# Optimization experiments

Hardware: AMD Instinct MI355X
Metric: run time of the kernel (lower is better)

The kernel has to match this reference:

```python
import jax, jax.numpy as jnp
from jax import lax
import numpy as np

C = 256
K = 3
PAD = 1


def _bilinear_sample(x, py, px):
    """Zero-padded bilinear sampling.
    x: [B,C,Hin,Win]; py,px: [B,Kt,H,W] float sample coords -> [B,C,Kt,H,W]."""
    B, Cc, Hin, Win = x.shape
    y0 = jnp.floor(py)
    x0 = jnp.floor(px)
    y1 = y0 + 1.0
    x1 = x0 + 1.0
    wy1 = py - y0
    wy0 = 1.0 - wy1
    wx1 = px - x0
    wx0 = 1.0 - wx1
    xf = x.reshape(B, Cc, Hin * Win)

    def corner(yi, xi, wy, wx):
        valid = (yi >= 0) & (yi < Hin) & (xi >= 0) & (xi < Win)
        yc = jnp.clip(yi, 0, Hin - 1).astype(jnp.int32)
        xc = jnp.clip(xi, 0, Win - 1).astype(jnp.int32)
        idx = yc * Win + xc  # [B,Kt,H,W]
        g = jax.vmap(lambda xb, ib: xb[:, ib])(xf, idx)  # [B,C,Kt,H,W]
        w = (wy * wx) * valid.astype(x.dtype)
        return g * w[:, None]

    return (corner(y0, x0, wy0, wx0) + corner(y0, x1, wy0, wx1)
            + corner(y1, x0, wy1, wx0) + corner(y1, x1, wy1, wx1))


def _arm_forward(x, w_off, b_off, w, b):
    B, Cc, H, W = x.shape
    # offset-predicting conv (standard 3x3, pad 1)
    off = lax.conv_general_dilated(
        x, w_off, window_strides=(1, 1), padding=[(PAD, PAD), (PAD, PAD)],
        dimension_numbers=('NCHW', 'OIHW', 'NCHW')) + b_off[None, :, None, None]
    off = off.reshape(B, K * K, 2, H, W)  # [:, k, 0]=dy, [:, k, 1]=dx (mmcv layout)
    ky, kx = jnp.meshgrid(jnp.arange(K), jnp.arange(K), indexing='ij')
    ky = ky.reshape(-1).astype(x.dtype)  # [9]
    kx = kx.reshape(-1).astype(x.dtype)
    base_y = jnp.arange(H, dtype=x.dtype)[None, None, :, None]
    base_x = jnp.arange(W, dtype=x.dtype)[None, None, None, :]
    py = base_y - PAD + ky[None, :, None, None] + off[:, :, 0]  # [B,9,H,W]
    px = base_x - PAD + kx[None, :, None, None] + off[:, :, 1]
    sampled = _bilinear_sample(x, py, px)  # [B,C,9,H,W]
    out = jnp.einsum('bckhw,ock->bohw', sampled, w.reshape(Cc, Cc, K * K))
    out = out + b[None, :, None, None]
    return jax.nn.sigmoid(out)


def setup_inputs() -> dict:
    key = jax.random.key(0)
    k1, k2, k3, k4 = jax.random.split(key, 4)
    B, H, W = 8, 64, 64
    x = jax.random.normal(k1, (B, C, H, W), dtype=jnp.float32)
    # offset conv params (mmcv zero-inits these; use small random to exercise sampling)
    w_off = jax.random.normal(k2, (2 * K * K, C, K, K), dtype=jnp.float32) * 0.01
    b_off = jnp.zeros((2 * K * K,), dtype=jnp.float32)
    # deformable conv weight/bias (kaiming-ish scale)
    scale = 1.0 / np.sqrt(C * K * K)
    w = jax.random.normal(k3, (C, C, K, K), dtype=jnp.float32) * scale
    b = jax.random.normal(k4, (C,), dtype=jnp.float32) * scale
    return {"Fstagei": x, "w_off": w_off, "b_off": b_off, "w": w, "b": b}


def reference(Fstagei, w_off, b_off, w, b):
    return _arm_forward(Fstagei, w_off, b_off, w, b)
```

## Files before the change

kernel.cpp:

```cpp
#include <hip/hip_runtime.h>

typedef unsigned short u16;
typedef unsigned int u32;
typedef __attribute__((ext_vector_type(8))) short short8;
typedef __attribute__((ext_vector_type(4))) float f32x4;

#define BB 8
#define CCH 256
#define HH 64
#define WW 64
#define HP 66
#define NPOS 4096
#define KTOT 2304

#define XT_BYTES   17842176ull
#define W2R_OFF    17842176ull
#define WOFF2_OFF  19021824ull
#define OFF2_OFF   40402944ull
#define WS_MIN     42762240ull

__device__ __forceinline__ u16 f2bf(float f) {
    union { float f; u32 u; } v; v.f = f;
    u32 r = v.u + 0x7FFFu + ((v.u >> 16) & 1u);
    return (u16)(r >> 16);
}
__device__ __forceinline__ u32 pk2(float a, float b) {
    return (u32)f2bf(a) | ((u32)f2bf(b) << 16);
}
__device__ __forceinline__ u32 cvtpk(float lo, float hi) {
    u32 r;
    asm("v_cvt_pk_bf16_f32 %0, %1, %2" : "=v"(r) : "v"(lo), "v"(hi));
    return r;
}
__device__ __forceinline__ void bf2x2(u32 p, float& a, float& b) {
    union { u32 u; float f; } va, vb;
    va.u = p << 16; vb.u = p & 0xffff0000u;
    a = va.f; b = vb.f;
}
__device__ __forceinline__ void ldg_lds16(const u16* g, u16* l) {
    __builtin_amdgcn_global_load_lds((const __attribute__((address_space(1))) u32*)g,
                                     (__attribute__((address_space(3))) u32*)l, 16, 0, 0);
}

__global__ __launch_bounds__(256) void k_pre(const float* __restrict__ w, const float* __restrict__ w_off,
                                             const float* __restrict__ x,
                                             u16* __restrict__ W2r, u16* __restrict__ Woff2,
                                             u16* __restrict__ xT) {
    __shared__ __align__(16) float SH[4608];
    int bx = blockIdx.x;
    int t = threadIdx.x;
    if (bx < 256) {
        int o = bx;
        const float* src = w + (size_t)o * 2304;
#pragma unroll
        for (int j = 0; j < 9; ++j) SH[j * 256 + t] = src[j * 256 + t];
        __syncthreads();
        u16* dst = W2r + (size_t)o * 2304;
#pragma unroll
        for (int k = 0; k < 9; ++k) dst[k * 256 + t] = f2bf(SH[t * 9 + k]);
    } else if (bx == 256) {
        for (int o2 = 0; o2 < 32; ++o2) {
            if (o2 < 18) {
                const float* src = w_off + (size_t)o2 * 2304;
#pragma unroll
                for (int j = 0; j < 9; ++j) SH[j * 256 + t] = src[j * 256 + t];
                __syncthreads();
#pragma unroll
                for (int k = 0; k < 9; ++k) Woff2[(size_t)o2 * 2304 + k * 256 + t] = f2bf(SH[t * 9 + k]);
                __syncthreads();
            } else {
#pragma unroll
                for (int k = 0; k < 9; ++k) Woff2[(size_t)o2 * 2304 + k * 256 + t] = 0;
            }
        }
    } else if (bx < 777) {
        int idx = (bx - 257) * 4 + (t >> 6);
        int b = idx / 260, m = idx - b * 260;
        int y, xx;
        if (m < 66)       { y = 0;  xx = m; }
        else if (m < 132) { y = 65; xx = m - 66; }
        else if (m < 196) { y = m - 132 + 1; xx = 0; }
        else              { y = m - 196 + 1; xx = 65; }
        u16* p = xT + ((size_t)(b * HP + y) * HP + xx) * CCH + (t & 63) * 4;
        uint2 zz; zz.x = 0; zz.y = 0;
        *(uint2*)p = zz;
    } else {
        int idx = bx - 777;
        int b = idx & 7;
        int r = idx >> 3;
        int y = r & 63, c0 = (r >> 6) * 64;
        {
            int i = t >> 2, seg = t & 3;
            const float* src = x + (((size_t)(b * CCH + c0 + i) * HH + y) * WW) + seg * 16;
            float4 v0 = *(const float4*)(src);
            float4 v1 = *(const float4*)(src + 4);
            float4 v2 = *(const float4*)(src + 8);
            float4 v3 = *(const float4*)(src + 12);
            *(float4*)&SH[i * 72 + seg * 16]      = v0;
            *(float4*)&SH[i * 72 + seg * 16 + 4]  = v1;
            *(float4*)&SH[i * 72 + seg * 16 + 8]  = v2;
            *(float4*)&SH[i * 72 + seg * 16 + 12] = v3;
        }
        __syncthreads();
        {
            int xc = t >> 2, cs = t & 3;
            u16* dst = xT + (((size_t)(b * HP + y + 1) * HP) + (xc + 1)) * CCH + c0 + cs * 16;
            u32 p[8];
#pragma unroll
            for (int j = 0; j < 8; ++j)
                p[j] = pk2(SH[(cs * 16 + 2 * j) * 72 + xc], SH[(cs * 16 + 2 * j + 1) * 72 + xc]);
            uint4 d0, d1;
            d0.x = p[0]; d0.y = p[1]; d0.z = p[2]; d0.w = p[3];
            d1.x = p[4]; d1.y = p[5]; d1.z = p[6]; d1.w = p[7];
            *(uint4*)dst = d0;
            *(uint4*)(dst + 8) = d1;
        }
    }
}

__global__ __launch_bounds__(256) void k_off2(const u16* __restrict__ xT,
                                              const u16* __restrict__ Woff2,
                                              const float* __restrict__ b_off,
                                              float2* __restrict__ off2) {
    __shared__ __align__(16) u16 AS[3][2048];
    __shared__ __align__(16) u16 BS[3][8192];
    int b = blockIdx.x;
    int pos0 = blockIdx.y * 128;
    int t = threadIdx.x, lane = t & 63, wv = t >> 6;

    int srow = lane >> 3;
    int sw8 = ((lane & 7) ^ srow) << 3;
    const u16* pXb = xT + (size_t)b * HP * HP * CCH;

    f32x4 acc[2][2];
    f32x4 z = {0.f, 0.f, 0.f, 0.f};
    acc[0][0] = z; acc[0][1] = z; acc[1][0] = z; acc[1][1] = z;

    auto stage = [&](int gs, int d) {
        int t9 = gs >> 2, cs = gs & 3;
        int ky = t9 / 3, kx = t9 - (t9 / 3) * 3;
        int koff = t9 * 256 + cs * 64;
        {
            int row = wv * 8 + srow;
            ldg_lds16(Woff2 + (size_t)row * KTOT + koff + sw8, &AS[d][wv * 512]);
        }
#pragma unroll
        for (int i = 0; i < 4; ++i) {
            int inst = wv * 4 + i;
            int rowg = pos0 + inst * 8 + srow;
            int py_ = rowg >> 6, px_ = rowg & 63;
            const u16* g = pXb + (((size_t)(py_ + ky) * HP) + px_ + kx) * CCH + cs * 64 + sw8;
            ldg_lds16(g, &BS[d][inst * 512]);
        }
    };

    stage(0, 0);
    stage(1, 1);

    int m = lane & 15, q = lane >> 4, key = lane & 7;
    for (int gs = 0; gs < 36; ++gs) {
        int cur = gs % 3;
        if (gs <= 34) { asm volatile("s_waitcnt vmcnt(5)" ::: "memory"); }
        else          { asm volatile("s_waitcnt vmcnt(0)" ::: "memory"); }
        __builtin_amdgcn_s_barrier();
        if (gs < 34) stage(gs + 2, (gs + 2) % 3);
#pragma unroll
        for (int j = 0; j < 2; ++j) {
            int slot8 = (((j * 4 + q) ^ key) << 3);
            short8 a0 = *(const short8*)&AS[cur][m * 64 + slot8];
            short8 a1 = *(const short8*)&AS[cur][(16 + m) * 64 + slot8];
            short8 b0 = *(const short8*)&BS[cur][(wv * 32 + m) * 64 + slot8];
            short8 b1 = *(const short8*)&BS[cur][(wv * 32 + 16 + m) * 64 + slot8];
            acc[0][0] = __builtin_amdgcn_mfma_f32_16x16x32_bf16(a0, b0, acc[0][0], 0, 0, 0);
            acc[0][1] = __builtin_amdgcn_mfma_f32_16x16x32_bf16(a0, b1, acc[0][1], 0, 0, 0);
            acc[1][0] = __builtin_amdgcn_mfma_f32_16x16x32_bf16(a1, b0, acc[1][0], 0, 0, 0);
            acc[1][1] = __builtin_amdgcn_mfma_f32_16x16x32_bf16(a1, b1, acc[1][1], 0, 0, 0);
        }
        asm volatile("s_waitcnt lgkmcnt(0)" ::: "memory");
    }

    int nn = lane & 15;
#pragma unroll
    for (int ao = 0; ao < 2; ++ao)
#pragma unroll
        for (int bn = 0; bn < 2; ++bn) {
            int pos = pos0 + wv * 32 + bn * 16 + nn;
#pragma unroll
            for (int rp = 0; rp < 2; ++rp) {
                int o = ao * 16 + q * 4 + rp * 2;
                if (o < 18) {
                    float2 v;
                    v.x = acc[ao][bn][rp * 2]     + b_off[o];
                    v.y = acc[ao][bn][rp * 2 + 1] + b_off[o + 1];
                    off2[(((size_t)(b * 9 + (o >> 1))) << 12) + pos] = v;
                }
            }
        }
}

__global__ __launch_bounds__(512, 2) void k_gemm(const u16* __restrict__ xT,
                                                 const float2* __restrict__ off2,
                                                 const u16* __restrict__ W2r,
                                                 const float* __restrict__ bias,
                                                 float* __restrict__ out) {
    __shared__ __align__(16) u16 AS[2][16384];
    __shared__ __align__(16) u16 BSF[128 * 264];
    int b = blockIdx.x;
    int pos0 = blockIdx.z * 128;
    int t = threadIdx.x, lane = t & 63, wv = t >> 6;
    int wr = wv >> 1, wc = wv & 1;

    int srow = lane >> 3;
    int sw8 = ((lane & 7) ^ srow) << 3;
    const u16* pA = W2r;

    int brow0 = t >> 3;
    int bcl = (t & 7) << 3;
    int bbase = b * HP * HP;

    f32x4 acc[4][4];
    f32x4 z = {0.f, 0.f, 0.f, 0.f};
#pragma unroll
    for (int i = 0; i < 4; ++i)
#pragma unroll
        for (int j = 0; j < 4; ++j) acc[i][j] = z;

    auto stageA = [&](int gs, int d) {
        int k9 = gs >> 2, cs = gs & 3;
        int koffA = k9 * 256 + cs * 64;
#pragma unroll
        for (int i = 0; i < 4; ++i) {
            int inst = wv * 4 + i;
            int row = inst * 8 + srow;
            ldg_lds16(pA + (size_t)row * KTOT + koffA + sw8, &AS[d][inst * 512]);
        }
    };

    const u16* gp[2][4];
    float wt[2][4];
    float2 fnext[2];
    uint4 gv[8];

    auto computeState = [&](int tap) {
#pragma unroll
        for (int ii = 0; ii < 2; ++ii) {
            int pos = pos0 + brow0 + (ii << 6);
            int y = pos >> 6, x = pos & 63;
            int ky = tap / 3, kx = tap - (tap / 3) * 3;
            float pyf = (float)(y - 1 + ky) + fnext[ii].x;
            float pxf = (float)(x - 1 + kx) + fnext[ii].y;
            float y0f = floorf(pyf), x0f = floorf(pxf);
            int y0 = (int)y0f, x0 = (int)x0f;
            int y1 = y0 + 1, x1 = x0 + 1;
            float wy1 = pyf - y0f, wy0 = 1.f - wy1;
            float wx1 = pxf - x0f, wx0 = 1.f - wx1;
            bool vy0 = (y0 >= 0) & (y0 < HH), vy1 = (y1 >= 0) & (y1 < HH);
            bool vx0 = (x0 >= 0) & (x0 < WW), vx1 = (x1 >= 0) & (x1 < WW);
            int yc0 = min(max(y0, 0), HH - 1), yc1 = min(max(y1, 0), HH - 1);
            int xc0 = min(max(x0, 0), WW - 1), xc1 = min(max(x1, 0), WW - 1);
            wt[ii][0] = (vy0 & vx0) ? wy0 * wx0 : 0.f;
            wt[ii][1] = (vy0 & vx1) ? wy0 * wx1 : 0.f;
            wt[ii][2] = (vy1 & vx0) ? wy1 * wx0 : 0.f;
            wt[ii][3] = (vy1 & vx1) ? wy1 * wx1 : 0.f;
            gp[ii][0] = xT + (size_t)(bbase + (yc0 + 1) * HP + xc0 + 1) * CCH + bcl;
            gp[ii][1] = xT + (size_t)(bbase + (yc0 + 1) * HP + xc1 + 1) * CCH + bcl;
            gp[ii][2] = xT + (size_t)(bbase + (yc1 + 1) * HP + xc0 + 1) * CCH + bcl;
            gp[ii][3] = xT + (size_t)(bbase + (yc1 + 1) * HP + xc1 + 1) * CCH + bcl;
        }
    };
    auto gatherRegion = [&](int rr) {
#pragma unroll
        for (int ii = 0; ii < 2; ++ii)
#pragma unroll
            for (int c = 0; c < 4; ++c)
                gv[ii * 4 + c] = *(const uint4*)(gp[ii][c] + rr * 64);
    };
    auto blendWrite = [&](int rr) {
#pragma unroll
        for (int ii = 0; ii < 2; ++ii) {
            int row = brow0 + (ii << 6);
            float v[8];
#pragma unroll
            for (int dw = 0; dw < 4; ++dw) {
                float a0, b0_, a1, b1_, a2, b2_, a3, b3_;
                bf2x2(((const u32*)&gv[ii * 4 + 0])[dw], a0, b0_);
                bf2x2(((const u32*)&gv[ii * 4 + 1])[dw], a1, b1_);
                bf2x2(((const u32*)&gv[ii * 4 + 2])[dw], a2, b2_);
                bf2x2(((const u32*)&gv[ii * 4 + 3])[dw], a3, b3_);
                v[2 * dw]     = wt[ii][0] * a0 + wt[ii][1] * a1 + wt[ii][2] * a2 + wt[ii][3] * a3;
                v[2 * dw + 1] = wt[ii][0] * b0_ + wt[ii][1] * b1_ + wt[ii][2] * b2_ + wt[ii][3] * b3_;
            }
            uint4 sv;
            sv.x = cvtpk(v[0], v[1]); sv.y = cvtpk(v[2], v[3]);
            sv.z = cvtpk(v[4], v[5]); sv.w = cvtpk(v[6], v[7]);
            *(uint4*)&BSF[row * 264 + rr * 64 + bcl] = sv;
        }
    };

    {
        fnext[0] = off2[((size_t)(b * 9 + 0) << 12) + pos0 + brow0];
        fnext[1] = off2[((size_t)(b * 9 + 0) << 12) + pos0 + brow0 + 64];
        computeState(0);
#pragma unroll
        for (int rr = 0; rr < 4; ++rr) {
            gatherRegion(rr);
            blendWrite(rr);
        }
        fnext[0] = off2[((size_t)(b * 9 + 1) << 12) + pos0 + brow0];
        fnext[1] = off2[((size_t)(b * 9 + 1) << 12) + pos0 + brow0 + 64];
        stageA(0, 0);
        asm volatile("s_waitcnt lgkmcnt(0)" ::: "memory");
    }

    int m = lane & 15, q = lane >> 4, key = lane & 7;
    for (int gs = 0; gs <= 35; ++gs) {
        int t9 = gs >> 2, cs = gs & 3, cur = gs & 1;
        if (gs >= 1 && gs <= 32) { asm volatile("s_waitcnt vmcnt(8)" ::: "memory"); }
        else                     { asm volatile("s_waitcnt vmcnt(0)" ::: "memory"); }
        __builtin_amdgcn_s_barrier();

        if (gs < 35) stageA(gs + 1, cur ^ 1);
        __builtin_amdgcn_sched_barrier(0);

        if (gs >= 1 && gs <= 32) {
            asm volatile("s_waitcnt vmcnt(4)" ::: "memory");
            blendWrite((cs + 3) & 3);
        }
        if (cs == 0 && t9 <= 7) computeState(t9 + 1);
        if (gs <= 31) {
            if (cs == 3 && t9 <= 6) {
                fnext[0] = off2[((size_t)(b * 9 + t9 + 2) << 12) + pos0 + brow0];
                fnext[1] = off2[((size_t)(b * 9 + t9 + 2) << 12) + pos0 + brow0 + 64];
            }
            gatherRegion(cs);
        }
        __builtin_amdgcn_sched_barrier(0);

#pragma unroll
        for (int j = 0; j < 2; ++j) {
            int slot8 = (((j * 4 + q) ^ key) << 3);
            int bchunk = (cs * 8 + j * 4 + q) << 3;
            short8 af[4], bfr[4];
#pragma unroll
            for (int ao = 0; ao < 4; ++ao)
                af[ao] = *(const short8*)&AS[cur][(wr * 64 + ao * 16 + m) * 64 + slot8];
#pragma unroll
            for (int bn = 0; bn < 4; ++bn)
                bfr[bn] = *(const short8*)&BSF[(wc * 64 + bn * 16 + m) * 264 + bchunk];
            __builtin_amdgcn_s_setprio(1);
#pragma unroll
            for (int ao = 0; ao < 4; ++ao)
#pragma unroll
                for (int bn = 0; bn < 4; ++bn)
                    acc[ao][bn] = __builtin_amdgcn_mfma_f32_16x16x32_bf16(af[ao], bfr[bn], acc[ao][bn], 0, 0, 0);
            __builtin_amdgcn_s_setprio(0);
        }
        asm volatile("s_waitcnt lgkmcnt(0)" ::: "memory");
    }

    int nn = lane & 15;
#pragma unroll
    for (int ao = 0; ao < 4; ++ao) {
        int ob = wr * 64 + ao * 16 + q * 4;
#pragma unroll
        for (int bn = 0; bn < 4; ++bn) {
            int pos = pos0 + wc * 64 + bn * 16 + nn;
#pragma unroll
            for (int r = 0; r < 4; ++r) {
                float v = acc[ao][bn][r] + bias[ob + r];
                float sg = 1.0f / (1.0f + __expf(-v));
                out[(size_t)((b * CCH + ob + r) * NPOS) + pos] = sg;
            }
        }
    }
}

extern "C" void kernel_launch(void* const* d_in, const int* in_sizes, int n_in,
                              void* d_out, int out_size, void* d_ws, size_t ws_size,
                              hipStream_t stream) {
    const float* x     = (const float*)d_in[0];
    const float* w_off = (const float*)d_in[1];
    const float* b_off = (const float*)d_in[2];
    const float* w     = (const float*)d_in[3];
    const float* bias  = (const float*)d_in[4];
    float* out = (float*)d_out;

    char* ws = (char*)d_ws;
    u16*    xT    = (u16*)ws;
    u16*    W2r   = (u16*)(ws + W2R_OFF);
    u16*    Woff2 = (u16*)(ws + WOFF2_OFF);
    float2* off2  = (float2*)(ws + OFF2_OFF);

    if (ws_size < WS_MIN) return;

    k_pre<<<2825, 256, 0, stream>>>(w, w_off, x, W2r, Woff2, xT);
    k_off2<<<dim3(8, 32), 256, 0, stream>>>(xT, Woff2, b_off, off2);
    k_gemm<<<dim3(8, 1, 32), 512, 0, stream>>>(xT, off2, W2r, bias, out);
}
```

Before: 193.0 us.

## Pre-swizzle weights into MFMA fragment layout and load A directly from global

The preprocessing kernel now writes the deformable-conv weights in a layout that matches the MFMA A-fragment order, one 16-byte chunk per lane. The GEMM kernel loads A fragments straight from global/L2 into registers, dropping the LDS staging buffer and its double buffering. The position tile per block is halved to 64, and the grid doubles with a higher occupancy hint. This shrinks LDS use and adds parallelism, but the global A loads have no explicit prefetch and the shared weights are read more often overall.

```diff
diff --git a/kernel.cpp b/kernel.cpp
--- a/kernel.cpp
+++ b/kernel.cpp
@@ -55,9 +55,20 @@
 #pragma unroll
         for (int j = 0; j < 9; ++j) SH[j * 256 + t] = src[j * 256 + t];
         __syncthreads();
-        u16* dst = W2r + (size_t)o * 2304;
-#pragma unroll
-        for (int k = 0; k < 9; ++k) dst[k * 256 + t] = f2bf(SH[t * 9 + k]);
+        int m = o & 15, ao = (o >> 4) & 3, wr = o >> 6;
+        for (int ci = t; ci < 288; ci += 256) {
+            int gs = ci >> 3, jj = (ci >> 2) & 1, q = ci & 3;
+            int kbase = gs * 64 + (jj * 4 + q) * 8;
+            int tap = kbase >> 8, ch0 = kbase & 255;
+            uint4 sv;
+            sv.x = pk2(SH[(ch0 + 0) * 9 + tap], SH[(ch0 + 1) * 9 + tap]);
+            sv.y = pk2(SH[(ch0 + 2) * 9 + tap], SH[(ch0 + 3) * 9 + tap]);
+            sv.z = pk2(SH[(ch0 + 4) * 9 + tap], SH[(ch0 + 5) * 9 + tap]);
+            sv.w = pk2(SH[(ch0 + 6) * 9 + tap], SH[(ch0 + 7) * 9 + tap]);
+            u16* dst = W2r + ((size_t)((((gs * 2 + jj) * 4 + wr) << 2) + ao) << 9)
+                           + ((q * 16 + m) << 3);
+            *(uint4*)dst = sv;
+        }
     } else if (bx == 256) {
         for (int o2 = 0; o2 < 32; ++o2) {
             if (o2 < 18) {
@@ -198,161 +209,125 @@
         }
 }
 
-__global__ __launch_bounds__(512, 2) void k_gemm(const u16* __restrict__ xT,
+__global__ __launch_bounds__(512, 4) void k_gemm(const u16* __restrict__ xT,
                                                  const float2* __restrict__ off2,
-                                                 const u16* __restrict__ W2r,
+                                                 const u16* __restrict__ W2rf,
                                                  const float* __restrict__ bias,
                                                  float* __restrict__ out) {
-    __shared__ __align__(16) u16 AS[2][16384];
-    __shared__ __align__(16) u16 BSF[128 * 264];
+    __shared__ __align__(16) u16 BSF[64 * 264];
     int b = blockIdx.x;
-    int pos0 = blockIdx.z * 128;
+    int pos0 = blockIdx.z * 64;
     int t = threadIdx.x, lane = t & 63, wv = t >> 6;
     int wr = wv >> 1, wc = wv & 1;
 
-    int srow = lane >> 3;
-    int sw8 = ((lane & 7) ^ srow) << 3;
-    const u16* pA = W2r;
-
-    int brow0 = t >> 3;
+    int brow = t >> 3;
     int bcl = (t & 7) << 3;
     int bbase = b * HP * HP;
 
-    f32x4 acc[4][4];
+    f32x4 acc[4][2];
     f32x4 z = {0.f, 0.f, 0.f, 0.f};
 #pragma unroll
-    for (int i = 0; i < 4; ++i)
-#pragma unroll
-        for (int j = 0; j < 4; ++j) acc[i][j] = z;
-
-    auto stageA = [&](int gs, int d) {
-        int k9 = gs >> 2, cs = gs & 3;
-        int koffA = k9 * 256 + cs * 64;
-#pragma unroll
-        for (int i = 0; i < 4; ++i) {
-            int inst = wv * 4 + i;
-            int row = inst * 8 + srow;
-            ldg_lds16(pA + (size_t)row * KTOT + koffA + sw8, &AS[d][inst * 512]);
-        }
-    };
-
-    const u16* gp[2][4];
-    float wt[2][4];
-    float2 fnext[2];
-    uint4 gv[8];
+    for (int i = 0; i < 4; ++i) { acc[i][0] = z; acc[i][1] = z; }
+
+    const u16* gp[4];
+    float wt[4];
+    float2 fnext;
+    uint4 gv[4];
 
     auto computeState = [&](int tap) {
-#pragma unroll
-        for (int ii = 0; ii < 2; ++ii) {
-            int pos = pos0 + brow0 + (ii << 6);
-            int y = pos >> 6, x = pos & 63;
-            int ky = tap / 3, kx = tap - (tap / 3) * 3;
-            float pyf = (float)(y - 1 + ky) + fnext[ii].x;
-            float pxf = (float)(x - 1 + kx) + fnext[ii].y;
-            float y0f = floorf(pyf), x0f = floorf(pxf);
-            int y0 = (int)y0f, x0 = (int)x0f;
-            int y1 = y0 + 1, x1 = x0 + 1;
-            float wy1 = pyf - y0f, wy0 = 1.f - wy1;
-            float wx1 = pxf - x0f, wx0 = 1.f - wx1;
-            bool vy0 = (y0 >= 0) & (y0 < HH), vy1 = (y1 >= 0) & (y1 < HH);
-            bool vx0 = (x0 >= 0) & (x0 < WW), vx1 = (x1 >= 0) & (x1 < WW);
-            int yc0 = min(max(y0, 0), HH - 1), yc1 = min(max(y1, 0), HH - 1);
-            int xc0 = min(max(x0, 0), WW - 1), xc1 = min(max(x1, 0), WW - 1);
-            wt[ii][0] = (vy0 & vx0) ? wy0 * wx0 : 0.f;
-            wt[ii][1] = (vy0 & vx1) ? wy0 * wx1 : 0.f;
-            wt[ii][2] = (vy1 & vx0) ? wy1 * wx0 : 0.f;
-            wt[ii][3] = (vy1 & vx1) ? wy1 * wx1 : 0.f;
-            gp[ii][0] = xT + (size_t)(bbase + (yc0 + 1) * HP + xc0 + 1) * CCH + bcl;
-            gp[ii][1] = xT + (size_t)(bbase + (yc0 + 1) * HP + xc1 + 1) * CCH + bcl;
-            gp[ii][2] = xT + (size_t)(bbase + (yc1 + 1) * HP + xc0 + 1) * CCH + bcl;
-            gp[ii][3] = xT + (size_t)(bbase + (yc1 + 1) * HP + xc1 + 1) * CCH + bcl;
-        }
+        int pos = pos0 + brow;
+        int y = pos >> 6, x = pos & 63;
+        int ky = tap / 3, kx = tap - (tap / 3) * 3;
+        float pyf = (float)(y - 1 + ky) + fnext.x;
+        float pxf = (float)(x - 1 + kx) + fnext.y;
+        float y0f = floorf(pyf), x0f = floorf(pxf);
+        int y0 = (int)y0f, x0 = (int)x0f;
+        int y1 = y0 + 1, x1 = x0 + 1;
+        float wy1 = pyf - y0f, wy0 = 1.f - wy1;
+        float wx1 = pxf - x0f, wx0 = 1.f - wx1;
+        bool vy0 = (y0 >= 0) & (y0 < HH), vy1 = (y1 >= 0) & (y1 < HH);
+        bool vx0 = (x0 >= 0) & (x0 < WW), vx1 = (x1 >= 0) & (x1 < WW);
+        int yc0 = min(max(y0, 0), HH - 1), yc1 = min(max(y1, 0), HH - 1);
+        int xc0 = min(max(x0, 0), WW - 1), xc1 = min(max(x1, 0), WW - 1);
+        wt[0] = (vy0 & vx0) ? wy0 * wx0 : 0.f;
+        wt[1] = (vy0 & vx1) ? wy0 * wx1 : 0.f;
+        wt[2] = (vy1 & vx0) ? wy1 * wx0 : 0.f;
+        wt[3] = (vy1 & vx1) ? wy1 * wx1 : 0.f;
+        gp[0] = xT + (size_t)(bbase + (yc0 + 1) * HP + xc0 + 1) * CCH + bcl;
+        gp[1] = xT + (size_t)(bbase + (yc0 + 1) * HP + xc1 + 1) * CCH + bcl;
+        gp[2] = xT + (size_t)(bbase + (yc1 + 1) * HP + xc0 + 1) * CCH + bcl;
+        gp[3] = xT + (size_t)(bbase + (yc1 + 1) * HP + xc1 + 1) * CCH + bcl;
     };
     auto gatherRegion = [&](int rr) {
 #pragma unroll
-        for (int ii = 0; ii < 2; ++ii)
-#pragma unroll
-            for (int c = 0; c < 4; ++c)
-                gv[ii * 4 + c] = *(const uint4*)(gp[ii][c] + rr * 64);
+        for (int c = 0; c < 4; ++c)
+            gv[c] = *(const uint4*)(gp[c] + rr * 64);
     };
     auto blendWrite = [&](int rr) {
-#pragma unroll
-        for (int ii = 0; ii < 2; ++ii) {
-            int row = brow0 + (ii << 6);
-            float v[8];
-#pragma unroll
-            for (int dw = 0; dw < 4; ++dw) {
-                float a0, b0_, a1, b1_, a2, b2_, a3, b3_;
-                bf2x2(((const u32*)&gv[ii * 4 + 0])[dw], a0, b0_);
-                bf2x2(((const u32*)&gv[ii * 4 + 1])[dw], a1, b1_);
-                bf2x2(((const u32*)&gv[ii * 4 + 2])[dw], a2, b2_);
-                bf2x2(((const u32*)&gv[ii * 4 + 3])[dw], a3, b3_);
-                v[2 * dw]     = wt[ii][0] * a0 + wt[ii][1] * a1 + wt[ii][2] * a2 + wt[ii][3] * a3;
-                v[2 * dw + 1] = wt[ii][0] * b0_ + wt[ii][1] * b1_ + wt[ii][2] * b2_ + wt[ii][3] * b3_;
-            }
-            uint4 sv;
-            sv.x = cvtpk(v[0], v[1]); sv.y = cvtpk(v[2], v[3]);
-            sv.z = cvtpk(v[4], v[5]); sv.w = cvtpk(v[6], v[7]);
-            *(uint4*)&BSF[row * 264 + rr * 64 + bcl] = sv;
-        }
+        float v[8];
+#pragma unroll
+        for (int dw = 0; dw < 4; ++dw) {
+            float a0, b0_, a1, b1_, a2, b2_, a3, b3_;
+            bf2x2(((const u32*)&gv[0])[dw], a0, b0_);
+            bf2x2(((const u32*)&gv[1])[dw], a1, b1_);
+            bf2x2(((const u32*)&gv[2])[dw], a2, b2_);
+            bf2x2(((const u32*)&gv[3])[dw], a3, b3_);
+            v[2 * dw]     = wt[0] * a0 + wt[1] * a1 + wt[2] * a2 + wt[3] * a3;
+            v[2 * dw + 1] = wt[0] * b0_ + wt[1] * b1_ + wt[2] * b2_ + wt[3] * b3_;
+        }
+        uint4 sv;
+        sv.x = cvtpk(v[0], v[1]); sv.y = cvtpk(v[2], v[3]);
+        sv.z = cvtpk(v[4], v[5]); sv.w = cvtpk(v[6], v[7]);
+        *(uint4*)&BSF[brow * 264 + rr * 64 + bcl] = sv;
     };
 
     {
-        fnext[0] = off2[((size_t)(b * 9 + 0) << 12) + pos0 + brow0];
-        fnext[1] = off2[((size_t)(b * 9 + 0) << 12) + pos0 + brow0 + 64];
+        fnext = off2[((size_t)(b * 9) << 12) + pos0 + brow];
         computeState(0);
 #pragma unroll
         for (int rr = 0; rr < 4; ++rr) {
             gatherRegion(rr);
             blendWrite(rr);
         }
-        fnext[0] = off2[((size_t)(b * 9 + 1) << 12) + pos0 + brow0];
-        fnext[1] = off2[((size_t)(b * 9 + 1) << 12) + pos0 + brow0 + 64];
-        stageA(0, 0);
+        fnext = off2[((size_t)(b * 9 + 1) << 12) + pos0 + brow];
         asm volatile("s_waitcnt lgkmcnt(0)" ::: "memory");
     }
 
-    int m = lane & 15, q = lane >> 4, key = lane & 7;
+    int m = lane & 15, q = lane >> 4;
     for (int gs = 0; gs <= 35; ++gs) {
-        int t9 = gs >> 2, cs = gs & 3, cur = gs & 1;
-        if (gs >= 1 && gs <= 32) { asm volatile("s_waitcnt vmcnt(8)" ::: "memory"); }
-        else                     { asm volatile("s_waitcnt vmcnt(0)" ::: "memory"); }
+        int t9 = gs >> 2, cs = gs & 3;
         __builtin_amdgcn_s_barrier();
 
-        if (gs < 35) stageA(gs + 1, cur ^ 1);
+        short8 af[8];
+#pragma unroll
+        for (int jj = 0; jj < 2; ++jj)
+#pragma unroll
+            for (int ao = 0; ao < 4; ++ao)
+                af[jj * 4 + ao] = *(const short8*)(W2rf
+                    + ((size_t)((((gs * 2 + jj) * 4 + wr) << 2) + ao) << 9) + (lane << 3));
         __builtin_amdgcn_sched_barrier(0);
 
-        if (gs >= 1 && gs <= 32) {
-            asm volatile("s_waitcnt vmcnt(4)" ::: "memory");
-            blendWrite((cs + 3) & 3);
-        }
+        if (gs >= 1 && gs <= 32) blendWrite((cs + 3) & 3);
         if (cs == 0 && t9 <= 7) computeState(t9 + 1);
         if (gs <= 31) {
-            if (cs == 3 && t9 <= 6) {
-                fnext[0] = off2[((size_t)(b * 9 + t9 + 2) << 12) + pos0 + brow0];
-                fnext[1] = off2[((size_t)(b * 9 + t9 + 2) << 12) + pos0 + brow0 + 64];
+            if (cs == 3 && t9 <= 6)
+                fnext = off2[((size_t)(b * 9 + t9 + 2) << 12) + pos0 + brow];
+            gatherRegion(cs);
+        }
+        __builtin_amdgcn_sched_barrier(0);
+
+#pragma unroll
+        for (int jj = 0; jj < 2; ++jj) {
+            int bchunk = (cs * 8 + jj * 4 + q) << 3;
+            short8 bfr[2];
+            bfr[0] = *(const short8*)&BSF[(wc * 32 + m) * 264 + bchunk];
+            bfr[1] = *(const short8*)&BSF[(wc * 32 + 16 + m) * 264 + bchunk];
+            __builtin_amdgcn_s_setprio(1);
+#pragma unroll
+            for (int ao = 0; ao < 4; ++ao) {
+                acc[ao][0] = __builtin_amdgcn_mfma_f32_16x16x32_bf16(af[jj * 4 + ao], bfr[0], acc[ao][0], 0, 0, 0);
+                acc[ao][1] = __builtin_amdgcn_mfma_f32_16x16x32_bf16(af[jj * 4 + ao], bfr[1], acc[ao][1], 0, 0, 0);
             }
-            gatherRegion(cs);
-        }
-        __builtin_amdgcn_sched_barrier(0);
-
-#pragma unroll
-        for (int j = 0; j < 2; ++j) {
-            int slot8 = (((j * 4 + q) ^ key) << 3);
-            int bchunk = (cs * 8 + j * 4 + q) << 3;
-            short8 af[4], bfr[4];
-#pragma unroll
-            for (int ao = 0; ao < 4; ++ao)
-                af[ao] = *(const short8*)&AS[cur][(wr * 64 + ao * 16 + m) * 64 + slot8];
-#pragma unroll
-            for (int bn = 0; bn < 4; ++bn)
-                bfr[bn] = *(const short8*)&BSF[(wc * 64 + bn * 16 + m) * 264 + bchunk];
-            __builtin_amdgcn_s_setprio(1);
-#pragma unroll
-            for (int ao = 0; ao < 4; ++ao)
-#pragma unroll
-                for (int bn = 0; bn < 4; ++bn)
-                    acc[ao][bn] = __builtin_amdgcn_mfma_f32_16x16x32_bf16(af[ao], bfr[bn], acc[ao][bn], 0, 0, 0);
             __builtin_amdgcn_s_setprio(0);
         }
         asm volatile("s_waitcnt lgkmcnt(0)" ::: "memory");
@@ -363,8 +338,8 @@
     for (int ao = 0; ao < 4; ++ao) {
         int ob = wr * 64 + ao * 16 + q * 4;
 #pragma unroll
-        for (int bn = 0; bn < 4; ++bn) {
-            int pos = pos0 + wc * 64 + bn * 16 + nn;
+        for (int bn = 0; bn < 2; ++bn) {
+            int pos = pos0 + wc * 32 + bn * 16 + nn;
 #pragma unroll
             for (int r = 0; r < 4; ++r) {
                 float v = acc[ao][bn][r] + bias[ob + r];
@@ -395,5 +370,5 @@
 
     k_pre<<<2825, 256, 0, stream>>>(w, w_off, x, W2r, Woff2, xT);
     k_off2<<<dim3(8, 32), 256, 0, stream>>>(xT, Woff2, b_off, off2);
-    k_gemm<<<dim3(8, 1, 32), 512, 0, stream>>>(xT, off2, W2r, bias, out);
-}
+    k_gemm<<<dim3(8, 1, 64), 512, 0, stream>>>(xT, off2, W2r, bias, out);
+}
```

After: 196.8 us. No clear change (+1.9%).

## Prepack weights in MFMA fragment order and load A directly into registers

Applied to the files above, without the earlier changes.

The pre-kernel now writes the bf16 deformable-conv weights in the exact per-lane MFMA fragment layout. The GEMM kernel then drops the LDS staging buffer for A and loads fragments straight from global memory into registers, double-buffered across two unrolled steps. This removes the LDS traffic and the explicit vmcnt waits for A, and frees 64KB of shared memory. In exchange it adds more VGPR pressure and relies on the compiler's implicit waits for global loads, which could stall the MFMAs.

```diff
diff --git a/kernel.cpp b/kernel.cpp
--- a/kernel.cpp
+++ b/kernel.cpp
@@ -55,9 +55,20 @@
 #pragma unroll
         for (int j = 0; j < 9; ++j) SH[j * 256 + t] = src[j * 256 + t];
         __syncthreads();
-        u16* dst = W2r + (size_t)o * 2304;
-#pragma unroll
-        for (int k = 0; k < 9; ++k) dst[k * 256 + t] = f2bf(SH[t * 9 + k]);
+        int m = o & 15, ao = (o >> 4) & 3, wr = o >> 6;
+        for (int ci = t; ci < 288; ci += 256) {
+            int gs = ci >> 3, jj = (ci >> 2) & 1, q = ci & 3;
+            int kbase = gs * 64 + (jj * 4 + q) * 8;
+            int tap = kbase >> 8, ch0 = kbase & 255;
+            uint4 sv;
+            sv.x = pk2(SH[(ch0 + 0) * 9 + tap], SH[(ch0 + 1) * 9 + tap]);
+            sv.y = pk2(SH[(ch0 + 2) * 9 + tap], SH[(ch0 + 3) * 9 + tap]);
+            sv.z = pk2(SH[(ch0 + 4) * 9 + tap], SH[(ch0 + 5) * 9 + tap]);
+            sv.w = pk2(SH[(ch0 + 6) * 9 + tap], SH[(ch0 + 7) * 9 + tap]);
+            u16* dst = W2r + ((size_t)((((gs * 2 + jj) * 4 + wr) << 2) + ao) << 9)
+                           + ((q * 16 + m) << 3);
+            *(uint4*)dst = sv;
+        }
     } else if (bx == 256) {
         for (int o2 = 0; o2 < 32; ++o2) {
             if (o2 < 18) {
@@ -200,20 +211,15 @@
 
 __global__ __launch_bounds__(512, 2) void k_gemm(const u16* __restrict__ xT,
                                                  const float2* __restrict__ off2,
-                                                 const u16* __restrict__ W2r,
+                                                 const u16* __restrict__ W2rf,
                                                  const float* __restrict__ bias,
                                                  float* __restrict__ out) {
-    __shared__ __align__(16) u16 AS[2][16384];
     __shared__ __align__(16) u16 BSF[128 * 264];
     int b = blockIdx.x;
     int pos0 = blockIdx.z * 128;
     int t = threadIdx.x, lane = t & 63, wv = t >> 6;
     int wr = wv >> 1, wc = wv & 1;
 
-    int srow = lane >> 3;
-    int sw8 = ((lane & 7) ^ srow) << 3;
-    const u16* pA = W2r;
-
     int brow0 = t >> 3;
     int bcl = (t & 7) << 3;
     int bbase = b * HP * HP;
@@ -224,17 +230,6 @@
     for (int i = 0; i < 4; ++i)
 #pragma unroll
         for (int j = 0; j < 4; ++j) acc[i][j] = z;
-
-    auto stageA = [&](int gs, int d) {
-        int k9 = gs >> 2, cs = gs & 3;
-        int koffA = k9 * 256 + cs * 64;
-#pragma unroll
-        for (int i = 0; i < 4; ++i) {
-            int inst = wv * 4 + i;
-            int row = inst * 8 + srow;
-            ldg_lds16(pA + (size_t)row * KTOT + koffA + sw8, &AS[d][inst * 512]);
-        }
-    };
 
     const u16* gp[2][4];
     float wt[2][4];
@@ -296,6 +291,16 @@
             *(uint4*)&BSF[row * 264 + rr * 64 + bcl] = sv;
         }
     };
+    auto loadA = [&](int gs, short8 (&af)[8]) {
+#pragma unroll
+        for (int jj = 0; jj < 2; ++jj)
+#pragma unroll
+            for (int ao = 0; ao < 4; ++ao)
+                af[jj * 4 + ao] = *(const short8*)(W2rf
+                    + ((size_t)((((gs * 2 + jj) * 4 + wr) << 2) + ao) << 9) + (lane << 3));
+    };
+
+    short8 afA[8], afB[8];
 
     {
         fnext[0] = off2[((size_t)(b * 9 + 0) << 12) + pos0 + brow0];
@@ -308,24 +313,17 @@
         }
         fnext[0] = off2[((size_t)(b * 9 + 1) << 12) + pos0 + brow0];
         fnext[1] = off2[((size_t)(b * 9 + 1) << 12) + pos0 + brow0 + 64];
-        stageA(0, 0);
+        loadA(0, afA);
         asm volatile("s_waitcnt lgkmcnt(0)" ::: "memory");
     }
 
-    int m = lane & 15, q = lane >> 4, key = lane & 7;
-    for (int gs = 0; gs <= 35; ++gs) {
-        int t9 = gs >> 2, cs = gs & 3, cur = gs & 1;
-        if (gs >= 1 && gs <= 32) { asm volatile("s_waitcnt vmcnt(8)" ::: "memory"); }
-        else                     { asm volatile("s_waitcnt vmcnt(0)" ::: "memory"); }
+    int m = lane & 15, q = lane >> 4;
+
+    auto body = [&](int gs, short8 (&cur)[8], short8 (&nxt)[8]) {
+        int t9 = gs >> 2, cs = gs & 3;
         __builtin_amdgcn_s_barrier();
 
-        if (gs < 35) stageA(gs + 1, cur ^ 1);
-        __builtin_amdgcn_sched_barrier(0);
-
-        if (gs >= 1 && gs <= 32) {
-            asm volatile("s_waitcnt vmcnt(4)" ::: "memory");
-            blendWrite((cs + 3) & 3);
-        }
+        if (gs >= 1 && gs <= 32) blendWrite((cs + 3) & 3);
         if (cs == 0 && t9 <= 7) computeState(t9 + 1);
         if (gs <= 31) {
             if (cs == 3 && t9 <= 6) {
@@ -334,16 +332,13 @@
             }
             gatherRegion(cs);
         }
+        if (gs < 35) loadA(gs + 1, nxt);
         __builtin_amdgcn_sched_barrier(0);
 
 #pragma unroll
-        for (int j = 0; j < 2; ++j) {
-            int slot8 = (((j * 4 + q) ^ key) << 3);
-            int bchunk = (cs * 8 + j * 4 + q) << 3;
-            short8 af[4], bfr[4];
-#pragma unroll
-            for (int ao = 0; ao < 4; ++ao)
-                af[ao] = *(const short8*)&AS[cur][(wr * 64 + ao * 16 + m) * 64 + slot8];
+        for (int jj = 0; jj < 2; ++jj) {
+            int bchunk = (cs * 8 + jj * 4 + q) << 3;
+            short8 bfr[4];
 #pragma unroll
             for (int bn = 0; bn < 4; ++bn)
                 bfr[bn] = *(const short8*)&BSF[(wc * 64 + bn * 16 + m) * 264 + bchunk];
@@ -352,10 +347,15 @@
             for (int ao = 0; ao < 4; ++ao)
 #pragma unroll
                 for (int bn = 0; bn < 4; ++bn)
-                    acc[ao][bn] = __builtin_amdgcn_mfma_f32_16x16x32_bf16(af[ao], bfr[bn], acc[ao][bn], 0, 0, 0);
+                    acc[ao][bn] = __builtin_amdgcn_mfma_f32_16x16x32_bf16(cur[jj * 4 + ao], bfr[bn], acc[ao][bn], 0, 0, 0);
             __builtin_amdgcn_s_setprio(0);
         }
         asm volatile("s_waitcnt lgkmcnt(0)" ::: "memory");
+    };
+
+    for (int gs = 0; gs < 36; gs += 2) {
+        body(gs, afA, afB);
+        body(gs + 1, afB, afA);
     }
 
     int nn = lane & 15;
```

New measurement: 202.4 us. +4.8%, slower.
